# Performance work log

Measured on AMD Instinct MI355X. Metric: run time of the kernel, lower is better.

## Reference

```python
import jax, jax.numpy as jnp
import numpy as np


def setup_inputs() -> dict:
    key = jax.random.key(0)
    k1, k2 = jax.random.split(key)
    x = jax.random.normal(k1, (16, 64, 224, 224), dtype=jnp.float32)
    # conv weight [out=1, in=2, kh=7, kw=7]; init roughly mimics small-normal init
    conv_w = jax.random.normal(k2, (1, 2, 7, 7), dtype=jnp.float32) * 0.01
    conv_b = jnp.zeros((1,), dtype=jnp.float32)
    return {"x": x, "conv_w": conv_w, "conv_b": conv_b}


def reference(x, conv_w, conv_b):
    # channel-wise mean and max -> [B, 2, H, W]
    avg_out = jnp.mean(x, axis=1, keepdims=True)
    max_out = jnp.max(x, axis=1, keepdims=True)
    feat = jnp.concatenate([avg_out, max_out], axis=1)
    # 2->1 channel 7x7 conv, padding 3 (same)
    y = jax.lax.conv_general_dilated(
        feat, conv_w,
        window_strides=(1, 1),
        padding=((3, 3), (3, 3)),
        dimension_numbers=("NCHW", "OIHW", "NCHW"),
    ) + conv_b[None, :, None, None]
    # sigmoid gate broadcast-multiplied back onto x
    return jax.nn.sigmoid(y) * x
```

## Files before the change

kernel.cpp:

```cpp
#include <hip/hip_runtime.h>
#include <math.h>

#define BB 16
#define CC 64
#define HH 224
#define WW 224
#define HWSZ (HH * WW)
#define HW4 (HWSZ / 4)
#define CHW4 (CC * HW4)

__global__ __launch_bounds__(256) void reduce_kernel(const float* __restrict__ x,
                                                     float* __restrict__ feat) {
    int idx = blockIdx.x * 256 + threadIdx.x;
    int b   = idx / HW4;
    int hw4 = idx - b * HW4;

    const float4* xp = reinterpret_cast<const float4*>(x) + (size_t)b * CHW4 + hw4;
    float4 v = xp[0];
    float4 s = v;
    float4 m = v;
#pragma unroll 8
    for (int c = 1; c < CC; ++c) {
        float4 t = xp[(size_t)c * HW4];
        s.x += t.x; s.y += t.y; s.z += t.z; s.w += t.w;
        m.x = fmaxf(m.x, t.x); m.y = fmaxf(m.y, t.y);
        m.z = fmaxf(m.z, t.z); m.w = fmaxf(m.w, t.w);
    }
    const float inv = 1.0f / 64.0f;
    s.x *= inv; s.y *= inv; s.z *= inv; s.w *= inv;

    float4* avgp = reinterpret_cast<float4*>(feat) + (size_t)b * 2 * HW4 + hw4;
    float4* maxp = avgp + HW4;
    *avgp = s;
    *maxp = m;
}

__global__ __launch_bounds__(256) void conv_kernel(const float* __restrict__ feat,
                                                   const float* __restrict__ cw,
                                                   const float* __restrict__ cb,
                                                   float* __restrict__ gate) {
    int idx = blockIdx.x * 256 + threadIdx.x;
    int b  = idx / HWSZ;
    int hw = idx - b * HWSZ;
    int h  = hw / WW;
    int w  = hw - h * WW;

    const float* fa = feat + (size_t)b * 2 * HWSZ;
    const float* fm = fa + HWSZ;

    float acc = cb[0];
#pragma unroll
    for (int kh = 0; kh < 7; ++kh) {
        int hh = h + kh - 3;
        if ((unsigned)hh >= (unsigned)HH) continue;
#pragma unroll
        for (int kw = 0; kw < 7; ++kw) {
            int ww = w + kw - 3;
            if ((unsigned)ww >= (unsigned)WW) continue;
            int o = hh * WW + ww;
            acc = fmaf(fa[o], cw[kh * 7 + kw], acc);
            acc = fmaf(fm[o], cw[49 + kh * 7 + kw], acc);
        }
    }
    gate[idx] = 1.0f / (1.0f + expf(-acc));
}

__global__ __launch_bounds__(256) void mul_kernel(const float* __restrict__ x,
                                                  const float* __restrict__ gate,
                                                  float* __restrict__ out) {
    int idx = blockIdx.x * 256 + threadIdx.x;
    int b   = idx / CHW4;
    int r   = idx - b * CHW4;
    int hw4 = r % HW4;

    float4 v = reinterpret_cast<const float4*>(x)[idx];
    float4 g = reinterpret_cast<const float4*>(gate)[(size_t)b * HW4 + hw4];
    v.x *= g.x; v.y *= g.y; v.z *= g.z; v.w *= g.w;
    reinterpret_cast<float4*>(out)[idx] = v;
}

extern "C" void kernel_launch(void* const* d_in, const int* in_sizes, int n_in,
                              void* d_out, int out_size, void* d_ws, size_t ws_size,
                              hipStream_t stream) {
    const float* x  = (const float*)d_in[0];
    const float* cw = (const float*)d_in[1];
    const float* cb = (const float*)d_in[2];
    float* out = (float*)d_out;

    float* feat = (float*)d_ws;
    float* gate = feat + (size_t)BB * 2 * HWSZ;

    reduce_kernel<<<(BB * HW4) / 256, 256, 0, stream>>>(x, feat);
    conv_kernel<<<(BB * HWSZ) / 256, 256, 0, stream>>>(feat, cw, cb, gate);
    mul_kernel<<<(BB * CHW4) / 256, 256, 0, stream>>>(x, gate, out);
}
```

Measured before the change: 414.4 us.

## Fuse reduce, conv and gating into one row-tiled kernel with shared memory

Replaces three kernels with a single kernel per (batch, 14-row tile). Each kernel computes channel mean/max including a 3-row halo into shared memory, runs the 7x7 conv plus sigmoid from shared memory, then multiplies x by the gate. This removes the global feature and gate buffers and two launches, and aims for cache reuse when x is re-read. In exchange it recomputes halo rows and runs only one 512-thread block per batch tile, which limits occupancy and serializes the phases.

```diff
diff --git a/kernel.cpp b/kernel.cpp
--- a/kernel.cpp
+++ b/kernel.cpp
@@ -7,76 +7,88 @@
 #define WW 224
 #define HWSZ (HH * WW)
 #define HW4 (HWSZ / 4)
-#define CHW4 (CC * HW4)
+#define R 14
+#define TILES (HH / R)
+#define FR (R + 6)
+#define FW 240
+#define W4 (WW / 4)
+#define T 512
 
-__global__ __launch_bounds__(256) void reduce_kernel(const float* __restrict__ x,
-                                                     float* __restrict__ feat) {
-    int idx = blockIdx.x * 256 + threadIdx.x;
-    int b   = idx / HW4;
-    int hw4 = idx - b * HW4;
+__global__ __launch_bounds__(T) void fused_kernel(const float* __restrict__ x,
+                                                  const float* __restrict__ cw,
+                                                  const float* __restrict__ cb,
+                                                  float* __restrict__ out) {
+    __shared__ float fa[FR * FW];
+    __shared__ float fm[FR * FW];
+    __shared__ alignas(16) float gate[R * WW];
+    __shared__ float wt[98];
 
-    const float4* xp = reinterpret_cast<const float4*>(x) + (size_t)b * CHW4 + hw4;
-    float4 v = xp[0];
-    float4 s = v;
-    float4 m = v;
+    const int blk = blockIdx.x;
+    const int b   = blk >> 4;
+    const int tb  = blk & 15;
+    const int h0  = tb * R;
+    const int t   = threadIdx.x;
+
+    for (int i = t; i < FR * FW; i += T) { fa[i] = 0.f; fm[i] = 0.f; }
+    if (t < 98) wt[t] = cw[t];
+    __syncthreads();
+
+    const float4* xb = reinterpret_cast<const float4*>(x) + (size_t)b * (CC * HW4);
+    for (int p = t; p < FR * W4; p += T) {
+        int pr = p / W4;
+        int pc = p - pr * W4;
+        int gh = h0 - 3 + pr;
+        if ((unsigned)gh >= (unsigned)HH) continue;
+        const float4* xp = xb + gh * W4 + pc;
+        float4 s = make_float4(0.f, 0.f, 0.f, 0.f);
+        float4 m = make_float4(-INFINITY, -INFINITY, -INFINITY, -INFINITY);
 #pragma unroll 8
-    for (int c = 1; c < CC; ++c) {
-        float4 t = xp[(size_t)c * HW4];
-        s.x += t.x; s.y += t.y; s.z += t.z; s.w += t.w;
-        m.x = fmaxf(m.x, t.x); m.y = fmaxf(m.y, t.y);
-        m.z = fmaxf(m.z, t.z); m.w = fmaxf(m.w, t.w);
+        for (int c = 0; c < CC; ++c) {
+            float4 u = xp[(size_t)c * HW4];
+            s.x += u.x; s.y += u.y; s.z += u.z; s.w += u.w;
+            m.x = fmaxf(m.x, u.x); m.y = fmaxf(m.y, u.y);
+            m.z = fmaxf(m.z, u.z); m.w = fmaxf(m.w, u.w);
+        }
+        const float inv = 1.0f / 64.0f;
+        int o = pr * FW + 3 + pc * 4;
+        fa[o + 0] = s.x * inv; fa[o + 1] = s.y * inv;
+        fa[o + 2] = s.z * inv; fa[o + 3] = s.w * inv;
+        fm[o + 0] = m.x; fm[o + 1] = m.y; fm[o + 2] = m.z; fm[o + 3] = m.w;
     }
-    const float inv = 1.0f / 64.0f;
-    s.x *= inv; s.y *= inv; s.z *= inv; s.w *= inv;
+    __syncthreads();
 
-    float4* avgp = reinterpret_cast<float4*>(feat) + (size_t)b * 2 * HW4 + hw4;
-    float4* maxp = avgp + HW4;
-    *avgp = s;
-    *maxp = m;
-}
+    const float bias = cb[0];
+    for (int p = t; p < R * WW; p += T) {
+        int r = p / WW;
+        int w = p - r * WW;
+        float acc = bias;
+#pragma unroll
+        for (int kh = 0; kh < 7; ++kh) {
+            int ro = (r + kh) * FW + w;
+#pragma unroll
+            for (int kw = 0; kw < 7; ++kw) {
+                acc = fmaf(fa[ro + kw], wt[kh * 7 + kw], acc);
+                acc = fmaf(fm[ro + kw], wt[49 + kh * 7 + kw], acc);
+            }
+        }
+        gate[p] = 1.0f / (1.0f + expf(-acc));
+    }
+    __syncthreads();
 
-__global__ __launch_bounds__(256) void conv_kernel(const float* __restrict__ feat,
-                                                   const float* __restrict__ cw,
-                                                   const float* __restrict__ cb,
-                                                   float* __restrict__ gate) {
-    int idx = blockIdx.x * 256 + threadIdx.x;
-    int b  = idx / HWSZ;
-    int hw = idx - b * HWSZ;
-    int h  = hw / WW;
-    int w  = hw - h * WW;
-
-    const float* fa = feat + (size_t)b * 2 * HWSZ;
-    const float* fm = fa + HWSZ;
-
-    float acc = cb[0];
-#pragma unroll
-    for (int kh = 0; kh < 7; ++kh) {
-        int hh = h + kh - 3;
-        if ((unsigned)hh >= (unsigned)HH) continue;
-#pragma unroll
-        for (int kw = 0; kw < 7; ++kw) {
-            int ww = w + kw - 3;
-            if ((unsigned)ww >= (unsigned)WW) continue;
-            int o = hh * WW + ww;
-            acc = fmaf(fa[o], cw[kh * 7 + kw], acc);
-            acc = fmaf(fm[o], cw[49 + kh * 7 + kw], acc);
-        }
+    float4* ob = reinterpret_cast<float4*>(out) + (size_t)b * (CC * HW4);
+    const float4* g4 = reinterpret_cast<const float4*>(gate);
+    const int NP = R * W4;
+    for (int i = t; i < CC * NP; i += T) {
+        int c  = i / NP;
+        int p  = i - c * NP;
+        int pr = p / W4;
+        int pc = p - pr * W4;
+        size_t off = (size_t)c * HW4 + (size_t)(h0 + pr) * W4 + pc;
+        float4 v = xb[off];
+        float4 g = g4[p];
+        v.x *= g.x; v.y *= g.y; v.z *= g.z; v.w *= g.w;
+        ob[off] = v;
     }
-    gate[idx] = 1.0f / (1.0f + expf(-acc));
-}
-
-__global__ __launch_bounds__(256) void mul_kernel(const float* __restrict__ x,
-                                                  const float* __restrict__ gate,
-                                                  float* __restrict__ out) {
-    int idx = blockIdx.x * 256 + threadIdx.x;
-    int b   = idx / CHW4;
-    int r   = idx - b * CHW4;
-    int hw4 = r % HW4;
-
-    float4 v = reinterpret_cast<const float4*>(x)[idx];
-    float4 g = reinterpret_cast<const float4*>(gate)[(size_t)b * HW4 + hw4];
-    v.x *= g.x; v.y *= g.y; v.z *= g.z; v.w *= g.w;
-    reinterpret_cast<float4*>(out)[idx] = v;
 }
 
 extern "C" void kernel_launch(void* const* d_in, const int* in_sizes, int n_in,
@@ -87,10 +99,5 @@
     const float* cb = (const float*)d_in[2];
     float* out = (float*)d_out;
 
-    float* feat = (float*)d_ws;
-    float* gate = feat + (size_t)BB * 2 * HWSZ;
-
-    reduce_kernel<<<(BB * HW4) / 256, 256, 0, stream>>>(x, feat);
-    conv_kernel<<<(BB * HWSZ) / 256, 256, 0, stream>>>(feat, cw, cb, gate);
-    mul_kernel<<<(BB * CHW4) / 256, 256, 0, stream>>>(x, gate, out);
+    fused_kernel<<<BB * TILES, T, 0, stream>>>(x, cw, cb, out);
 }
```

After: 407.2 us. Within noise of the previous version (-1.7%).
